# Optimization experiments

Hardware: AMD Instinct MI355X
Metric: run time of the kernel (lower is better)

The kernel has to match this reference:

```python
import jax, jax.numpy as jnp
import numpy as np

FEATURE_DIM = 128
HIDDEN_DIM = 64
MAPPING_SIZE = 64
SCALE = 10.0
B, N, H, W = 8, 65536, 56, 56


def setup_inputs() -> dict:
    key = jax.random.key(0)
    ks = jax.random.split(key, 12)
    features = jax.random.normal(ks[0], (B, FEATURE_DIM, H, W), dtype=jnp.float32)
    # points in [-1, 1]^3
    points = jax.random.uniform(ks[1], (B, N, 3), dtype=jnp.float32, minval=-1.0, maxval=1.0)
    # realistic pinhole intrinsics for a 56x56 feature map
    k_mat = jnp.array([[56.0, 0.0, 28.0], [0.0, 56.0, 28.0], [0.0, 0.0, 1.0]], dtype=jnp.float32)
    k = jnp.broadcast_to(k_mat, (B, 3, 3))
    # extrinsics: identity rotation, translate z by 2 so points are in front of camera
    rt_mat = jnp.concatenate([jnp.eye(3, dtype=jnp.float32), jnp.array([[0.0], [0.0], [2.0]], dtype=jnp.float32)], axis=1)
    rt = jnp.broadcast_to(rt_mat, (B, 3, 4))
    # learned params
    B_gauss = jax.random.normal(ks[2], (MAPPING_SIZE, 3), dtype=jnp.float32) * SCALE
    input_dim = FEATURE_DIM + 2 * MAPPING_SIZE
    W1 = jax.random.normal(ks[3], (input_dim, HIDDEN_DIM), dtype=jnp.float32) * 0.05
    b1 = jnp.zeros((HIDDEN_DIM,), dtype=jnp.float32)
    W2 = jax.random.normal(ks[4], (HIDDEN_DIM, HIDDEN_DIM), dtype=jnp.float32) * 0.05
    b2 = jnp.zeros((HIDDEN_DIM,), dtype=jnp.float32)
    W3 = jax.random.normal(ks[5], (HIDDEN_DIM, HIDDEN_DIM), dtype=jnp.float32) * 0.05
    b3 = jnp.zeros((HIDDEN_DIM,), dtype=jnp.float32)
    W4 = jax.random.normal(ks[6], (HIDDEN_DIM, 1), dtype=jnp.float32) * 0.05
    b4 = jnp.zeros((1,), dtype=jnp.float32)
    return {"features": features, "points": points, "k": k, "rt": rt,
            "B_gauss": B_gauss, "W1": W1, "b1": b1, "W2": W2, "b2": b2,
            "W3": W3, "b3": b3, "W4": W4, "b4": b4}


def _grid_sample_bilinear_zeros(grid, x, y):
    # grid: (B, C, H, W); x, y: (B, N) pixel coords (align_corners=False already unnormalized)
    Bc, C, Hc, Wc = grid.shape
    g = jnp.transpose(grid, (0, 2, 3, 1))  # (B, H, W, C)
    x0 = jnp.floor(x)
    y0 = jnp.floor(y)
    wx1 = x - x0  # frac
    wy1 = y - y0
    wx0 = 1.0 - wx1
    wy0 = 1.0 - wy1
    x0i = x0.astype(jnp.int32)
    y0i = y0.astype(jnp.int32)
    bidx = jnp.arange(Bc, dtype=jnp.int32)[:, None]  # (B, 1)

    def gather(ix, iy):
        inb = ((ix >= 0) & (ix < Wc) & (iy >= 0) & (iy < Hc)).astype(grid.dtype)  # (B, N)
        vals = g[bidx, jnp.clip(iy, 0, Hc - 1), jnp.clip(ix, 0, Wc - 1)]  # (B, N, C)
        return vals * inb[..., None]

    out = (gather(x0i, y0i) * (wx0 * wy0)[..., None]
           + gather(x0i + 1, y0i) * (wx1 * wy0)[..., None]
           + gather(x0i, y0i + 1) * (wx0 * wy1)[..., None]
           + gather(x0i + 1, y0i + 1) * (wx1 * wy1)[..., None])
    return out  # (B, N, C)


def reference(features, points, k, rt, B_gauss, W1, b1, W2, b2, W3, b3, W4, b4):
    Bc, Nc, _ = points.shape
    Hc, Wc = features.shape[-2:]
    # --- camera projection ---
    homo = jnp.concatenate([points, jnp.ones((Bc, Nc, 1), dtype=points.dtype)], axis=2)  # (B,N,4)
    cam = jnp.einsum('bij,bnj->bni', rt, homo)   # (B,N,3)
    img = jnp.einsum('bij,bnj->bni', k, cam)     # (B,N,3)
    z = img[:, :, 2:3] + 1e-8
    uv = img[:, :, :2] / z
    valid = (img[:, :, 2:3] > 0).astype(points.dtype)  # (B,N,1)
    u_norm = (2.0 * uv[..., 0] + 1.0) / Wc - 1.0
    v_norm = (2.0 * uv[..., 1] + 1.0) / Hc - 1.0
    # grid_sample align_corners=False unnormalization: ix = ((g+1)*W - 1)/2
    x = ((u_norm + 1.0) * Wc - 1.0) * 0.5
    y = ((v_norm + 1.0) * Hc - 1.0) * 0.5
    img_feats = _grid_sample_bilinear_zeros(features, x, y) * valid  # (B,N,C)
    # --- Fourier mapping ---
    x_proj = (2.0 * np.pi) * jnp.einsum('bnd,md->bnm', points, B_gauss)  # (B,N,M)
    coord_feats = jnp.concatenate([jnp.sin(x_proj), jnp.cos(x_proj)], axis=-1)  # (B,N,2M)
    # --- MLP ---
    inp = jnp.concatenate([img_feats, coord_feats], axis=2)  # (B,N,C+2M)
    h = jax.nn.relu(inp @ W1 + b1)
    h = jax.nn.relu(h @ W2 + b2)
    h = jax.nn.relu(h @ W3 + b3)
    out = h @ W4 + b4  # (B,N,1)
    return out
```

## Files before the change

### kernel.cpp

```cpp
#include <hip/hip_runtime.h>

#define FDIM 128
#define HDIM 64
#define MSIZE 64
#define IMG_W 56
#define IMG_H 56
#define NPIX (IMG_W * IMG_H)
#define NB 8
#define NPTS 65536

typedef _Float16 f16x8 __attribute__((ext_vector_type(8)));
typedef __fp16 hf16x2 __attribute__((ext_vector_type(2)));
typedef float f32x4 __attribute__((ext_vector_type(4)));

#define W2_OFF 16384
#define W3_OFF 20480
#define BG_OFF 49152
#define FT_BYTE_OFF 50176
#define G_BYTE_OFF 6472704
#define TR16_BLOCKS (NPIX / 16 * NB)

__device__ __forceinline__ void lds_fence() {
    __asm__ volatile("s_waitcnt lgkmcnt(0)" ::: "memory");
}

__global__ __launch_bounds__(256) void prep_kernel(const float* __restrict__ in,
                                                   const float* __restrict__ W1,
                                                   const float* __restrict__ W2,
                                                   const float* __restrict__ W3,
                                                   const float* __restrict__ Bg,
                                                   _Float16* __restrict__ ws) {
    if (blockIdx.x < TR16_BLOCKS) {
        __shared__ float tile[16][133];
        _Float16* out = ws + FT_BYTE_OFF / 2;
        const int b = blockIdx.x / (NPIX / 16);
        const int pbase = (blockIdx.x % (NPIX / 16)) * 16;
        const int t = threadIdx.x;
        const float* src = in + (size_t)b * FDIM * NPIX;
        _Float16*    dst = out + (size_t)b * NPIX * FDIM;
        const int pq = t & 3;
        const int ch = t >> 2;
#pragma unroll
        for (int it = 0; it < 2; ++it) {
            const int c = it * 64 + ch;
            const float4 v = *(const float4*)(src + (size_t)c * NPIX + pbase + pq * 4);
            tile[pq * 4 + 0][c] = v.x;
            tile[pq * 4 + 1][c] = v.y;
            tile[pq * 4 + 2][c] = v.z;
            tile[pq * 4 + 3][c] = v.w;
        }
        __syncthreads();
        const int px = t >> 4;
        const int hk = (t & 15) * 8;
        union { f16x8 v; hf16x2 h[4]; } hv;
#pragma unroll
        for (int j = 0; j < 4; ++j)
            hv.h[j] = __builtin_amdgcn_cvt_pkrtz(tile[px][hk + 2 * j], tile[px][hk + 2 * j + 1]);
        *(f16x8*)(dst + (size_t)(pbase + px) * FDIM + hk) = hv.v;
    } else if (blockIdx.x < TR16_BLOCKS + 12) {
        const int t = (blockIdx.x - TR16_BLOCKS) * 256 + threadIdx.x;
        const int l = t & 63;
        const int q = l >> 4;
        const int col = l & 15;
        const int frag = t >> 6;
        if (frag < 32) {
            const int kt = frag >> 2, nt = frag & 3;
#pragma unroll
            for (int j = 0; j < 8; ++j) {
                int k = kt * 32 + q * 8 + j;
                int row = (k < 128) ? k : (128 + (k & 1) * 64 + ((k - 128) >> 1));
                ws[((size_t)(frag * 64 + l)) * 8 + j] = (_Float16)W1[row * HDIM + nt * 16 + col];
            }
        } else if (frag < 40) {
            const int f2 = frag - 32;
            const int kt = f2 >> 2, nt = f2 & 3;
#pragma unroll
            for (int j = 0; j < 8; ++j) {
                int row = kt * 32 + q * 8 + j;
                ws[W2_OFF + ((size_t)(f2 * 64 + l)) * 8 + j] = (_Float16)W2[row * HDIM + nt * 16 + col];
            }
        } else {
            const int f3 = frag - 40;
            const int kt = f3 >> 2, nt = f3 & 3;
#pragma unroll
            for (int j = 0; j < 8; ++j) {
                int row = kt * 32 + q * 8 + j;
                ws[W3_OFF + ((size_t)(f3 * 64 + l)) * 8 + j] = (_Float16)W3[row * HDIM + nt * 16 + col];
            }
        }
    } else {
        const int t = threadIdx.x;
        if (t < MSIZE) {
            float* bgs = (float*)((char*)ws + BG_OFF);
            bgs[t]       = Bg[t * 3 + 0];
            bgs[64 + t]  = Bg[t * 3 + 1];
            bgs[128 + t] = Bg[t * 3 + 2];
        }
    }
}

__global__ __launch_bounds__(256, 4) void gemm_g(_Float16* __restrict__ ws) {
    const int tid = threadIdx.x;
    const int wid = tid >> 6;
    const int l   = tid & 63;
    const int q   = l >> 4;
    const int col = l & 15;
    const int T = blockIdx.x * 4 + wid;
    const int b = T / (NPIX / 32);
    const int tile = T % (NPIX / 32);
    const int pbase = tile * 32;
    const _Float16* ft = ws + FT_BYTE_OFF / 2;
    _Float16* Gp = ws + G_BYTE_OFF / 2;
    const f32x4 zero4 = {0.0f, 0.0f, 0.0f, 0.0f};
    f32x4 acc[2][4];
#pragma unroll
    for (int mt = 0; mt < 2; ++mt)
#pragma unroll
        for (int nt = 0; nt < 4; ++nt) acc[mt][nt] = zero4;
#pragma unroll
    for (int kt = 0; kt < 4; ++kt) {
        f16x8 bf[4];
#pragma unroll
        for (int nt = 0; nt < 4; ++nt)
            bf[nt] = *(const f16x8*)(ws + ((size_t)((kt * 4 + nt) * 64 + l)) * 8);
#pragma unroll
        for (int mt = 0; mt < 2; ++mt) {
            f16x8 af = *(const f16x8*)(ft + ((size_t)(b * NPIX + pbase + mt * 16 + col)) * FDIM
                                       + kt * 32 + q * 8);
#pragma unroll
            for (int nt = 0; nt < 4; ++nt)
                acc[mt][nt] = __builtin_amdgcn_mfma_f32_16x16x32_f16(af, bf[nt], acc[mt][nt], 0, 0, 0);
        }
    }
#pragma unroll
    for (int mt = 0; mt < 2; ++mt)
#pragma unroll
        for (int nt = 0; nt < 4; ++nt)
#pragma unroll
            for (int r = 0; r < 4; ++r)
                Gp[((size_t)(b * NPIX + pbase + mt * 16 + q * 4 + r)) * HDIM + nt * 16 + col]
                    = (_Float16)acc[mt][nt][r];
}

struct Rec {
    float w0[2], w1[2], w2[2], w3[2];
    int   i0[2], i1[2], i2[2], i3[2];
    float qx[2], qy[2], qz[2];
};

__device__ __forceinline__ void phaseF(f32x4 acc[2][4], const _Float16* __restrict__ w1l,
                                       const float* __restrict__ bgs, const Rec& R,
                                       int q, int l) {
#pragma unroll
    for (int ktf = 0; ktf < 4; ++ktf) {
        const f32x4 bgx = *(const f32x4*)(bgs + ktf * 16 + q * 4);
        const f32x4 bgy = *(const f32x4*)(bgs + 64 + ktf * 16 + q * 4);
        const f32x4 bgz = *(const f32x4*)(bgs + 128 + ktf * 16 + q * 4);
        f16x8 bf[4];
#pragma unroll
        for (int nt = 0; nt < 4; ++nt)
            bf[nt] = *(const f16x8*)(w1l + ((size_t)((ktf * 4 + nt) * 64 + l)) * 8);
#pragma unroll
        for (int mt = 0; mt < 2; ++mt) {
            union { f16x8 v; hf16x2 h[4]; } af;
#pragma unroll
            for (int i = 0; i < 4; ++i) {
                float t = bgx[i] * R.qx[mt] + bgy[i] * R.qy[mt] + bgz[i] * R.qz[mt];
                float tf = __builtin_amdgcn_fractf(t);
                af.h[i] = __builtin_amdgcn_cvt_pkrtz(__builtin_amdgcn_sinf(tf),
                                                     __builtin_amdgcn_cosf(tf));
            }
#pragma unroll
            for (int nt = 0; nt < 4; ++nt)
                acc[mt][nt] = __builtin_amdgcn_mfma_f32_16x16x32_f16(af.v, bf[nt], acc[mt][nt], 0, 0, 0);
        }
    }
}

__device__ __forceinline__ void mlp_tail2(f32x4 acc[2][4], _Float16* __restrict__ Ah,
                                          const _Float16* __restrict__ wfrag,
                                          const _Float16* __restrict__ Gp,
                                          const Rec& R,
                                          const float* __restrict__ b1,
                                          const float* __restrict__ b2,
                                          const float* __restrict__ b3,
                                          const float* __restrict__ W4,
                                          const float* __restrict__ b4,
                                          float* __restrict__ out, int outbase,
                                          int q, int col, int l) {
    const f32x4 zero4 = {0.0f, 0.0f, 0.0f, 0.0f};
    f16x8 g[2][2][4];
#pragma unroll
    for (int ktl = 0; ktl < 2; ++ktl)
#pragma unroll
        for (int mt = 0; mt < 2; ++mt) {
            const int co = ktl * 32 + q * 8;
            g[ktl][mt][0] = *(const f16x8*)(Gp + R.i0[mt] + co);
            g[ktl][mt][1] = *(const f16x8*)(Gp + R.i1[mt] + co);
            g[ktl][mt][2] = *(const f16x8*)(Gp + R.i2[mt] + co);
            g[ktl][mt][3] = *(const f16x8*)(Gp + R.i3[mt] + co);
        }
    f16x8 bfW[8];
#pragma unroll
    for (int f = 0; f < 8; ++f)
        bfW[f] = *(const f16x8*)(wfrag + W2_OFF + ((size_t)(f * 64 + l)) * 8);

    _Float16 wh[2][4];
#pragma unroll
    for (int mt = 0; mt < 2; ++mt) {
        wh[mt][0] = (_Float16)R.w0[mt]; wh[mt][1] = (_Float16)R.w1[mt];
        wh[mt][2] = (_Float16)R.w2[mt]; wh[mt][3] = (_Float16)R.w3[mt];
    }

    float bb[4];
#pragma unroll
    for (int nt = 0; nt < 4; ++nt) bb[nt] = b1[nt * 16 + col];
#pragma unroll
    for (int mt = 0; mt < 2; ++mt)
#pragma unroll
        for (int nt = 0; nt < 4; ++nt)
#pragma unroll
            for (int r = 0; r < 4; ++r)
                Ah[(mt * 16 + q * 4 + r) * 72 + nt * 16 + col]
                    = (_Float16)(acc[mt][nt][r] + bb[nt]);
    lds_fence();

#pragma unroll
    for (int mt = 0; mt < 2; ++mt)
#pragma unroll
        for (int nt = 0; nt < 4; ++nt) acc[mt][nt] = zero4;
#pragma unroll
    for (int ktl = 0; ktl < 2; ++ktl)
#pragma unroll
        for (int mt = 0; mt < 2; ++mt) {
            f16x8 af = *(const f16x8*)(&Ah[(mt * 16 + col) * 72 + ktl * 32 + q * 8]);
            af = af + g[ktl][mt][0] * wh[mt][0] + g[ktl][mt][1] * wh[mt][1]
                    + g[ktl][mt][2] * wh[mt][2] + g[ktl][mt][3] * wh[mt][3];
#pragma unroll
            for (int j = 0; j < 8; ++j)
                af[j] = af[j] > (_Float16)0.0f ? af[j] : (_Float16)0.0f;
#pragma unroll
            for (int nt = 0; nt < 4; ++nt)
                acc[mt][nt] = __builtin_amdgcn_mfma_f32_16x16x32_f16(af, bfW[ktl * 4 + nt], acc[mt][nt], 0, 0, 0);
        }

#pragma unroll
    for (int f = 0; f < 8; ++f)
        bfW[f] = *(const f16x8*)(wfrag + W3_OFF + ((size_t)(f * 64 + l)) * 8);

    lds_fence();
#pragma unroll
    for (int nt = 0; nt < 4; ++nt) bb[nt] = b2[nt * 16 + col];
#pragma unroll
    for (int mt = 0; mt < 2; ++mt)
#pragma unroll
        for (int nt = 0; nt < 4; ++nt)
#pragma unroll
            for (int r = 0; r < 4; ++r) {
                float hv = fmaxf(acc[mt][nt][r] + bb[nt], 0.0f);
                Ah[(mt * 16 + q * 4 + r) * 72 + nt * 16 + col] = (_Float16)hv;
            }
    lds_fence();

#pragma unroll
    for (int mt = 0; mt < 2; ++mt)
#pragma unroll
        for (int nt = 0; nt < 4; ++nt) acc[mt][nt] = zero4;
#pragma unroll
    for (int ktl = 0; ktl < 2; ++ktl)
#pragma unroll
        for (int mt = 0; mt < 2; ++mt) {
            f16x8 af = *(const f16x8*)(&Ah[(mt * 16 + col) * 72 + ktl * 32 + q * 8]);
#pragma unroll
            for (int nt = 0; nt < 4; ++nt)
                acc[mt][nt] = __builtin_amdgcn_mfma_f32_16x16x32_f16(af, bfW[ktl * 4 + nt], acc[mt][nt], 0, 0, 0);
        }

    float b3v[4], w4v[4];
#pragma unroll
    for (int nt = 0; nt < 4; ++nt) {
        b3v[nt] = b3[nt * 16 + col];
        w4v[nt] = W4[nt * 16 + col];
    }
    const float b4v = b4[0];
#pragma unroll
    for (int mt = 0; mt < 2; ++mt)
#pragma unroll
        for (int r = 0; r < 4; ++r) {
            float p = 0.0f;
#pragma unroll
            for (int nt = 0; nt < 4; ++nt)
                p = fmaf(fmaxf(acc[mt][nt][r] + b3v[nt], 0.0f), w4v[nt], p);
            p += __shfl_xor(p, 1);
            p += __shfl_xor(p, 2);
            p += __shfl_xor(p, 4);
            p += __shfl_xor(p, 8);
            if (col == 0) out[outbase + mt * 16 + q * 4 + r] = p + b4v;
        }
    lds_fence();
}

__global__ __launch_bounds__(256, 3) void decoder_mfma8(
    const _Float16* __restrict__ Gp,
    const float* __restrict__ points,
    const float* __restrict__ Kmat, const float* __restrict__ Rt,
    const _Float16* __restrict__ wfrag,
    const float* __restrict__ b1, const float* __restrict__ b2,
    const float* __restrict__ b3,
    const float* __restrict__ W4, const float* __restrict__ b4,
    float* __restrict__ out) {
    __shared__ _Float16 w1l[8192];
    __shared__ _Float16 lds[4 * 32 * 72];
    const int tid = threadIdx.x;
    const int wid = tid >> 6;
    const int l   = tid & 63;
    const int q   = l >> 4;
    const int col = l & 15;
    const int b     = blockIdx.x & 7;
    const int grp   = blockIdx.x >> 3;
    const int wbase = b * NPTS + grp * 256 + wid * 64;
    _Float16* Ah = lds + wid * 32 * 72;
    const float* bgs = (const float*)((const char*)wfrag + BG_OFF);

#pragma unroll
    for (int i = 0; i < 4; ++i)
        ((f16x8*)w1l)[i * 256 + tid] = ((const f16x8*)(wfrag + 8192))[i * 256 + tid];

    const int gid = wbase + l;
    const float px = points[(size_t)gid * 3 + 0];
    const float py = points[(size_t)gid * 3 + 1];
    const float pz = points[(size_t)gid * 3 + 2];
    const float* rt = Rt + b * 12;
    const float* km = Kmat + b * 9;
    float cx = rt[0] * px + rt[1] * py + rt[2]  * pz + rt[3];
    float cy = rt[4] * px + rt[5] * py + rt[6]  * pz + rt[7];
    float cz = rt[8] * px + rt[9] * py + rt[10] * pz + rt[11];
    float ix = km[0] * cx + km[1] * cy + km[2] * cz;
    float iy = km[3] * cx + km[4] * cy + km[5] * cz;
    float iz = km[6] * cx + km[7] * cy + km[8] * cz;
    float z  = iz + 1e-8f;
    float u  = ix / z;
    float v  = iy / z;
    float valid = (iz > 0.0f) ? 1.0f : 0.0f;
    float u_norm = (2.0f * u + 1.0f) / (float)IMG_W - 1.0f;
    float v_norm = (2.0f * v + 1.0f) / (float)IMG_H - 1.0f;
    float x = ((u_norm + 1.0f) * (float)IMG_W - 1.0f) * 0.5f;
    float y = ((v_norm + 1.0f) * (float)IMG_H - 1.0f) * 0.5f;
    float x0f = floorf(x), y0f = floorf(y);
    float wx1 = x - x0f, wy1 = y - y0f;
    float wx0 = 1.0f - wx1, wy0 = 1.0f - wy1;
    int x0 = (int)x0f, y0 = (int)y0f;
    int x1 = x0 + 1, y1 = y0 + 1;
    int x0c = x0 < 0 ? 0 : (x0 > IMG_W - 1 ? IMG_W - 1 : x0);
    int x1c = x1 < 0 ? 0 : (x1 > IMG_W - 1 ? IMG_W - 1 : x1);
    int y0c = y0 < 0 ? 0 : (y0 > IMG_H - 1 ? IMG_H - 1 : y0);
    int y1c = y1 < 0 ? 0 : (y1 > IMG_H - 1 ? IMG_H - 1 : y1);
    float mx0 = (x0 >= 0 && x0 < IMG_W) ? 1.0f : 0.0f;
    float mx1 = (x1 >= 0 && x1 < IMG_W) ? 1.0f : 0.0f;
    float my0 = (y0 >= 0 && y0 < IMG_H) ? 1.0f : 0.0f;
    float my1 = (y1 >= 0 && y1 < IMG_H) ? 1.0f : 0.0f;
    const int pb = b * NPIX;
    float r_w00 = wx0 * wy0 * mx0 * my0 * valid;
    float r_w10 = wx1 * wy0 * mx1 * my0 * valid;
    float r_w01 = wx0 * wy1 * mx0 * my1 * valid;
    float r_w11 = wx1 * wy1 * mx1 * my1 * valid;
    int r_i00 = (pb + y0c * IMG_W + x0c) * HDIM;
    int r_i10 = (pb + y0c * IMG_W + x1c) * HDIM;
    int r_i01 = (pb + y1c * IMG_W + x0c) * HDIM;
    int r_i11 = (pb + y1c * IMG_W + x1c) * HDIM;

    f32x4 acc[2][4];
    const f32x4 zero4 = {0.0f, 0.0f, 0.0f, 0.0f};

    {
        Rec R0;
#pragma unroll
        for (int mt = 0; mt < 2; ++mt) {
            const int src = mt * 16 + col;
            R0.w0[mt] = __shfl(r_w00, src);
            R0.w1[mt] = __shfl(r_w10, src);
            R0.w2[mt] = __shfl(r_w01, src);
            R0.w3[mt] = __shfl(r_w11, src);
            R0.i0[mt] = __shfl(r_i00, src);
            R0.i1[mt] = __shfl(r_i10, src);
            R0.i2[mt] = __shfl(r_i01, src);
            R0.i3[mt] = __shfl(r_i11, src);
            R0.qx[mt] = __shfl(px, src);
            R0.qy[mt] = __shfl(py, src);
            R0.qz[mt] = __shfl(pz, src);
        }
        __syncthreads();
#pragma unroll
        for (int mt = 0; mt < 2; ++mt)
#pragma unroll
            for (int nt = 0; nt < 4; ++nt) acc[mt][nt] = zero4;
        phaseF(acc, w1l, bgs, R0, q, l);
        mlp_tail2(acc, Ah, wfrag, Gp, R0, b1, b2, b3, W4, b4, out, wbase, q, col, l);
    }

    __builtin_amdgcn_sched_barrier(0);

    {
        Rec R1;
#pragma unroll
        for (int mt = 0; mt < 2; ++mt) {
            const int src = 32 + mt * 16 + col;
            R1.w0[mt] = __shfl(r_w00, src);
            R1.w1[mt] = __shfl(r_w10, src);
            R1.w2[mt] = __shfl(r_w01, src);
            R1.w3[mt] = __shfl(r_w11, src);
            R1.i0[mt] = __shfl(r_i00, src);
            R1.i1[mt] = __shfl(r_i10, src);
            R1.i2[mt] = __shfl(r_i01, src);
            R1.i3[mt] = __shfl(r_i11, src);
            R1.qx[mt] = __shfl(px, src);
            R1.qy[mt] = __shfl(py, src);
            R1.qz[mt] = __shfl(pz, src);
        }
#pragma unroll
        for (int mt = 0; mt < 2; ++mt)
#pragma unroll
            for (int nt = 0; nt < 4; ++nt) acc[mt][nt] = zero4;
        phaseF(acc, w1l, bgs, R1, q, l);
        mlp_tail2(acc, Ah, wfrag, Gp, R1, b1, b2, b3, W4, b4, out, wbase + 32, q, col, l);
    }
}

__global__ __launch_bounds__(64, 2) void decoder_valu(
    const float* __restrict__ feats, const float* __restrict__ points,
    const float* __restrict__ Kmat, const float* __restrict__ Rt,
    const float* __restrict__ Bg,
    const float* __restrict__ W1, const float* __restrict__ b1,
    const float* __restrict__ W2, const float* __restrict__ b2,
    const float* __restrict__ W3, const float* __restrict__ b3,
    const float* __restrict__ W4, const float* __restrict__ b4,
    float* __restrict__ out) {
    __shared__ float hbuf[64 * 65];
    const int tid = threadIdx.x;
    const int b   = blockIdx.x / (NPTS / 64);
    const int gid = blockIdx.x * 64 + tid;
    const float px = points[(size_t)gid * 3 + 0];
    const float py = points[(size_t)gid * 3 + 1];
    const float pz = points[(size_t)gid * 3 + 2];
    const float* rt = Rt + b * 12;
    const float* km = Kmat + b * 9;
    float cx = rt[0] * px + rt[1] * py + rt[2]  * pz + rt[3];
    float cy = rt[4] * px + rt[5] * py + rt[6]  * pz + rt[7];
    float cz = rt[8] * px + rt[9] * py + rt[10] * pz + rt[11];
    float ix = km[0] * cx + km[1] * cy + km[2] * cz;
    float iy = km[3] * cx + km[4] * cy + km[5] * cz;
    float iz = km[6] * cx + km[7] * cy + km[8] * cz;
    float z  = iz + 1e-8f;
    float u  = ix / z, v = iy / z;
    float valid = (iz > 0.0f) ? 1.0f : 0.0f;
    float u_norm = (2.0f * u + 1.0f) / (float)IMG_W - 1.0f;
    float v_norm = (2.0f * v + 1.0f) / (float)IMG_H - 1.0f;
    float x = ((u_norm + 1.0f) * (float)IMG_W - 1.0f) * 0.5f;
    float y = ((v_norm + 1.0f) * (float)IMG_H - 1.0f) * 0.5f;
    float x0f = floorf(x), y0f = floorf(y);
    float wx1 = x - x0f, wy1 = y - y0f;
    float wx0 = 1.0f - wx1, wy0 = 1.0f - wy1;
    int x0 = (int)x0f, y0 = (int)y0f;
    int x1 = x0 + 1, y1 = y0 + 1;
    int x0c = x0 < 0 ? 0 : (x0 > IMG_W - 1 ? IMG_W - 1 : x0);
    int x1c = x1 < 0 ? 0 : (x1 > IMG_W - 1 ? IMG_W - 1 : x1);
    int y0c = y0 < 0 ? 0 : (y0 > IMG_H - 1 ? IMG_H - 1 : y0);
    int y1c = y1 < 0 ? 0 : (y1 > IMG_H - 1 ? IMG_H - 1 : y1);
    float mx0 = (x0 >= 0 && x0 < IMG_W) ? 1.0f : 0.0f;
    float mx1 = (x1 >= 0 && x1 < IMG_W) ? 1.0f : 0.0f;
    float my0 = (y0 >= 0 && y0 < IMG_H) ? 1.0f : 0.0f;
    float my1 = (y1 >= 0 && y1 < IMG_H) ? 1.0f : 0.0f;
    float w00 = wx0 * wy0 * mx0 * my0 * valid;
    float w10 = wx1 * wy0 * mx1 * my0 * valid;
    float w01 = wx0 * wy1 * mx0 * my1 * valid;
    float w11 = wx1 * wy1 * mx1 * my1 * valid;
    float h[HDIM];
#pragma unroll
    for (int j = 0; j < HDIM; ++j) h[j] = b1[j];
    const float* fb = feats + (size_t)b * FDIM * NPIX;
    const int p00 = y0c * IMG_W + x0c, p10 = y0c * IMG_W + x1c;
    const int p01 = y1c * IMG_W + x0c, p11 = y1c * IMG_W + x1c;
#pragma unroll 1
    for (int c = 0; c < FDIM; ++c) {
        const float* fp = fb + (size_t)c * NPIX;
        float fv = w00 * fp[p00] + w10 * fp[p10] + w01 * fp[p01] + w11 * fp[p11];
        const float* wr = W1 + (size_t)c * HDIM;
#pragma unroll
        for (int j = 0; j < HDIM; ++j) h[j] = fmaf(fv, wr[j], h[j]);
    }
#pragma unroll 1
    for (int m = 0; m < MSIZE; ++m) {
        float t = Bg[m * 3 + 0] * px + Bg[m * 3 + 1] * py + Bg[m * 3 + 2] * pz;
        float tf = t - floorf(t);
        float s = __builtin_amdgcn_sinf(tf);
        float c = __builtin_amdgcn_cosf(tf);
        const float* wsn = W1 + (size_t)(FDIM + m) * HDIM;
        const float* wcs = W1 + (size_t)(FDIM + MSIZE + m) * HDIM;
#pragma unroll
        for (int j = 0; j < HDIM; ++j)
            h[j] = fmaf(s, wsn[j], fmaf(c, wcs[j], h[j]));
    }
    float* myh = &hbuf[tid * 65];
#pragma unroll
    for (int j = 0; j < HDIM; ++j) myh[j] = fmaxf(h[j], 0.0f);
    float h2[HDIM];
#pragma unroll
    for (int j = 0; j < HDIM; ++j) h2[j] = b2[j];
#pragma unroll 1
    for (int i = 0; i < HDIM; ++i) {
        float hi = myh[i];
        const float* wr = W2 + (size_t)i * HDIM;
#pragma unroll
        for (int j = 0; j < HDIM; ++j) h2[j] = fmaf(hi, wr[j], h2[j]);
    }
#pragma unroll
    for (int j = 0; j < HDIM; ++j) myh[j] = fmaxf(h2[j], 0.0f);
#pragma unroll
    for (int j = 0; j < HDIM; ++j) h[j] = b3[j];
#pragma unroll 1
    for (int i = 0; i < HDIM; ++i) {
        float hi = myh[i];
        const float* wr = W3 + (size_t)i * HDIM;
#pragma unroll
        for (int j = 0; j < HDIM; ++j) h[j] = fmaf(hi, wr[j], h[j]);
    }
    float acc = b4[0];
#pragma unroll
    for (int j = 0; j < HDIM; ++j) acc = fmaf(fmaxf(h[j], 0.0f), W4[j], acc);
    out[gid] = acc;
}

extern "C" void kernel_launch(void* const* d_in, const int* in_sizes, int n_in,
                              void* d_out, int out_size, void* d_ws, size_t ws_size,
                              hipStream_t stream) {
    const float* feats = (const float*)d_in[0];
    const float* pts   = (const float*)d_in[1];
    const float* k     = (const float*)d_in[2];
    const float* rt    = (const float*)d_in[3];
    const float* Bg    = (const float*)d_in[4];
    const float* W1    = (const float*)d_in[5];
    const float* b1    = (const float*)d_in[6];
    const float* W2    = (const float*)d_in[7];
    const float* b2    = (const float*)d_in[8];
    const float* W3    = (const float*)d_in[9];
    const float* b3    = (const float*)d_in[10];
    const float* W4    = (const float*)d_in[11];
    const float* b4    = (const float*)d_in[12];
    float* out = (float*)d_out;

    const size_t gBytes = (size_t)NB * NPIX * HDIM * sizeof(_Float16);
    const size_t need = G_BYTE_OFF + gBytes;

    if (ws_size >= need) {
        _Float16* wf = (_Float16*)d_ws;
        _Float16* Gp = (_Float16*)((char*)d_ws + G_BYTE_OFF);
        prep_kernel<<<TR16_BLOCKS + 13, 256, 0, stream>>>(feats, W1, W2, W3, Bg, wf);
        gemm_g<<<NB * NPIX / 32 / 4, 256, 0, stream>>>(wf);
        decoder_mfma8<<<NB * NPTS / 256, 256, 0, stream>>>(Gp, pts, k, rt, wf,
                                                           b1, b2, b3, W4, b4, out);
    } else {
        decoder_valu<<<NB * NPTS / 64, 64, 0, stream>>>(feats, pts, k, rt, Bg,
                                                        W1, b1, W2, b2, W3, b3, W4, b4, out);
    }
}
```

Before: 151.8 us.

## Fuse feature transpose into G projection GEMM and raise decoder occupancy

Removes the separate fp32-to-fp16 transpose pass over the feature map. The GEMM kernel now reads the channel-major fp32 features directly, converts them to fp16 in registers, and feeds them to MFMA over 16-pixel tiles. This drops a full intermediate write and read of the transposed feature buffer and shrinks the weight-pack kernel to 13 blocks. Separately, the decoder's launch bound goes from 3 to 4 blocks per CU, which may force register spills.

```diff
diff --git a/kernel.cpp b/kernel.cpp
--- a/kernel.cpp
+++ b/kernel.cpp
@@ -16,49 +16,19 @@
 #define W2_OFF 16384
 #define W3_OFF 20480
 #define BG_OFF 49152
-#define FT_BYTE_OFF 50176
-#define G_BYTE_OFF 6472704
-#define TR16_BLOCKS (NPIX / 16 * NB)
+#define G_BYTE_OFF 50176
 
 __device__ __forceinline__ void lds_fence() {
     __asm__ volatile("s_waitcnt lgkmcnt(0)" ::: "memory");
 }
 
-__global__ __launch_bounds__(256) void prep_kernel(const float* __restrict__ in,
-                                                   const float* __restrict__ W1,
+__global__ __launch_bounds__(256) void pack_kernel(const float* __restrict__ W1,
                                                    const float* __restrict__ W2,
                                                    const float* __restrict__ W3,
                                                    const float* __restrict__ Bg,
                                                    _Float16* __restrict__ ws) {
-    if (blockIdx.x < TR16_BLOCKS) {
-        __shared__ float tile[16][133];
-        _Float16* out = ws + FT_BYTE_OFF / 2;
-        const int b = blockIdx.x / (NPIX / 16);
-        const int pbase = (blockIdx.x % (NPIX / 16)) * 16;
-        const int t = threadIdx.x;
-        const float* src = in + (size_t)b * FDIM * NPIX;
-        _Float16*    dst = out + (size_t)b * NPIX * FDIM;
-        const int pq = t & 3;
-        const int ch = t >> 2;
-#pragma unroll
-        for (int it = 0; it < 2; ++it) {
-            const int c = it * 64 + ch;
-            const float4 v = *(const float4*)(src + (size_t)c * NPIX + pbase + pq * 4);
-            tile[pq * 4 + 0][c] = v.x;
-            tile[pq * 4 + 1][c] = v.y;
-            tile[pq * 4 + 2][c] = v.z;
-            tile[pq * 4 + 3][c] = v.w;
-        }
-        __syncthreads();
-        const int px = t >> 4;
-        const int hk = (t & 15) * 8;
-        union { f16x8 v; hf16x2 h[4]; } hv;
-#pragma unroll
-        for (int j = 0; j < 4; ++j)
-            hv.h[j] = __builtin_amdgcn_cvt_pkrtz(tile[px][hk + 2 * j], tile[px][hk + 2 * j + 1]);
-        *(f16x8*)(dst + (size_t)(pbase + px) * FDIM + hk) = hv.v;
-    } else if (blockIdx.x < TR16_BLOCKS + 12) {
-        const int t = (blockIdx.x - TR16_BLOCKS) * 256 + threadIdx.x;
+    if (blockIdx.x < 12) {
+        const int t = blockIdx.x * 256 + threadIdx.x;
         const int l = t & 63;
         const int q = l >> 4;
         const int col = l & 15;
@@ -99,47 +69,44 @@
     }
 }
 
-__global__ __launch_bounds__(256, 4) void gemm_g(_Float16* __restrict__ ws) {
+__global__ __launch_bounds__(256, 4) void feat2g(const float* __restrict__ in,
+                                                 const _Float16* __restrict__ ws,
+                                                 _Float16* __restrict__ Gp) {
     const int tid = threadIdx.x;
     const int wid = tid >> 6;
     const int l   = tid & 63;
     const int q   = l >> 4;
     const int col = l & 15;
     const int T = blockIdx.x * 4 + wid;
-    const int b = T / (NPIX / 32);
-    const int tile = T % (NPIX / 32);
-    const int pbase = tile * 32;
-    const _Float16* ft = ws + FT_BYTE_OFF / 2;
-    _Float16* Gp = ws + G_BYTE_OFF / 2;
+    const int b = T / (NPIX / 16);
+    const int tile = T % (NPIX / 16);
+    const int pbase = tile * 16;
+    const float* src = in + (size_t)b * FDIM * NPIX;
     const f32x4 zero4 = {0.0f, 0.0f, 0.0f, 0.0f};
-    f32x4 acc[2][4];
-#pragma unroll
-    for (int mt = 0; mt < 2; ++mt)
-#pragma unroll
-        for (int nt = 0; nt < 4; ++nt) acc[mt][nt] = zero4;
+    f32x4 acc[4];
+#pragma unroll
+    for (int nt = 0; nt < 4; ++nt) acc[nt] = zero4;
 #pragma unroll
     for (int kt = 0; kt < 4; ++kt) {
-        f16x8 bf[4];
-#pragma unroll
-        for (int nt = 0; nt < 4; ++nt)
-            bf[nt] = *(const f16x8*)(ws + ((size_t)((kt * 4 + nt) * 64 + l)) * 8);
-#pragma unroll
-        for (int mt = 0; mt < 2; ++mt) {
-            f16x8 af = *(const f16x8*)(ft + ((size_t)(b * NPIX + pbase + mt * 16 + col)) * FDIM
-                                       + kt * 32 + q * 8);
-#pragma unroll
-            for (int nt = 0; nt < 4; ++nt)
-                acc[mt][nt] = __builtin_amdgcn_mfma_f32_16x16x32_f16(af, bf[nt], acc[mt][nt], 0, 0, 0);
-        }
-    }
-#pragma unroll
-    for (int mt = 0; mt < 2; ++mt)
-#pragma unroll
-        for (int nt = 0; nt < 4; ++nt)
-#pragma unroll
-            for (int r = 0; r < 4; ++r)
-                Gp[((size_t)(b * NPIX + pbase + mt * 16 + q * 4 + r)) * HDIM + nt * 16 + col]
-                    = (_Float16)acc[mt][nt][r];
+        union { f16x8 v; hf16x2 h[4]; } af;
+#pragma unroll
+        for (int jj = 0; jj < 4; ++jj) {
+            float v0 = src[(size_t)(kt * 32 + q * 8 + 2 * jj)     * NPIX + pbase + col];
+            float v1 = src[(size_t)(kt * 32 + q * 8 + 2 * jj + 1) * NPIX + pbase + col];
+            af.h[jj] = __builtin_amdgcn_cvt_pkrtz(v0, v1);
+        }
+#pragma unroll
+        for (int nt = 0; nt < 4; ++nt) {
+            f16x8 bf = *(const f16x8*)(ws + ((size_t)((kt * 4 + nt) * 64 + l)) * 8);
+            acc[nt] = __builtin_amdgcn_mfma_f32_16x16x32_f16(af.v, bf, acc[nt], 0, 0, 0);
+        }
+    }
+#pragma unroll
+    for (int nt = 0; nt < 4; ++nt)
+#pragma unroll
+        for (int r = 0; r < 4; ++r)
+            Gp[((size_t)(b * NPIX + pbase + q * 4 + r)) * HDIM + nt * 16 + col]
+                = (_Float16)acc[nt][r];
 }
 
 struct Rec {
@@ -300,7 +267,7 @@
     lds_fence();
 }
 
-__global__ __launch_bounds__(256, 3) void decoder_mfma8(
+__global__ __launch_bounds__(256, 4) void decoder_mfma8(
     const _Float16* __restrict__ Gp,
     const float* __restrict__ points,
     const float* __restrict__ Kmat, const float* __restrict__ Rt,
@@ -554,8 +521,8 @@
     if (ws_size >= need) {
         _Float16* wf = (_Float16*)d_ws;
         _Float16* Gp = (_Float16*)((char*)d_ws + G_BYTE_OFF);
-        prep_kernel<<<TR16_BLOCKS + 13, 256, 0, stream>>>(feats, W1, W2, W3, Bg, wf);
-        gemm_g<<<NB * NPIX / 32 / 4, 256, 0, stream>>>(wf);
+        pack_kernel<<<13, 256, 0, stream>>>(W1, W2, W3, Bg, wf);
+        feat2g<<<NB * NPIX / 16 / 4, 256, 0, stream>>>(feats, wf, Gp);
         decoder_mfma8<<<NB * NPTS / 256, 256, 0, stream>>>(Gp, pts, k, rt, wf,
                                                            b1, b2, b3, W4, b4, out);
     } else {
```

New measurement: 163.0 us. +7.4%, slower.
